# Optimization experiments

Hardware: AMD Instinct MI355X
Metric: run time of the kernel (lower is better)

The kernel has to match this reference:

```python
import jax, jax.numpy as jnp
import numpy as np
from jax import lax

OBS, ACT, H, VOX = 2264, 32, 4096, 216  # voxel tail is 6*6*6


def _conv3d(v, w, b):
    # v: [1,1,6,6,6], w: [1,1,3,3,3] (OIDHW), SAME padding, stride 1
    y = lax.conv_general_dilated(v, w, window_strides=(1, 1, 1), padding='SAME',
                                 dimension_numbers=('NCDHW', 'OIDHW', 'NCDHW'))
    return jax.nn.relu(y + b.reshape(1, -1, 1, 1, 1))


def setup_inputs() -> dict:
    key = jax.random.key(0)
    ks = jax.random.split(key, 24)
    s = 0.05
    inp = {'x': jax.random.normal(ks[0], (1, OBS), dtype=jnp.float32)}
    # six Conv3d(1,1,3) kernels + biases
    for i in range(6):
        inp[f'cw{i}'] = jax.random.normal(ks[1 + i], (1, 1, 3, 3, 3), dtype=jnp.float32) * s
        inp[f'cb{i}'] = jax.random.normal(ks[7 + i], (1,), dtype=jnp.float32) * s
    # MLP: Linear(OBS->H), Linear(H->H), Linear(H->ACT); torch layout W:[out,in]
    inp['W0'] = jax.random.normal(ks[13], (H, OBS), dtype=jnp.float32) * 0.02
    inp['b0'] = jnp.zeros((H,), jnp.float32)
    inp['W1'] = jax.random.normal(ks[14], (H, H), dtype=jnp.float32) * 0.02
    inp['b1'] = jnp.zeros((H,), jnp.float32)
    inp['W2'] = jax.random.normal(ks[15], (ACT, H), dtype=jnp.float32) * 0.02
    inp['b2'] = jnp.zeros((ACT,), jnp.float32)
    # default transformations (in_shift=0, in_scale=1, out_shift=0, out_scale=1)
    inp['in_shift'] = jnp.zeros((OBS,), jnp.float32)
    inp['in_scale'] = jnp.ones((OBS,), jnp.float32)
    inp['out_shift'] = jnp.zeros((ACT,), jnp.float32)
    inp['out_scale'] = jnp.ones((ACT,), jnp.float32)
    return inp


def reference(x, cw0, cw1, cw2, cw3, cw4, cw5, cb0, cb1, cb2, cb3, cb4, cb5,
              W0, b0, W1, b1, W2, b2, in_shift, in_scale, out_shift, out_scale):
    v = x[:, -VOX:].reshape(1, 1, 6, 6, 6)
    for w, b in ((cw0, cb0), (cw1, cb1), (cw2, cb2), (cw3, cb3), (cw4, cb4), (cw5, cb5)):
        v = _conv3d(v, w, b)
    out = jnp.concatenate([x[:, :-VOX], v.reshape(1, VOX)], axis=1)
    out = (out - in_shift) / (in_scale + 1e-8)
    out = jnp.tanh(out @ W0.T + b0)
    out = jnp.tanh(out @ W1.T + b1)
    out = out @ W2.T + b2
    return out * out_scale + out_shift
```

## Files before the change

kernel.cpp:

```cpp
#include <hip/hip_runtime.h>
#include <math.h>

#define OBS 2264
#define ACT 32
#define HID 4096
#define VOX 216
#define PRE (OBS - VOX)
#define N4_OBS (OBS / 4)
#define N4_HID (HID / 4)
#define ROWS0 8
#define ROWS1 4

__global__ __launch_bounds__(256) void conv_norm_kernel(
    const float* __restrict__ x,
    const float* __restrict__ cw0, const float* __restrict__ cb0,
    const float* __restrict__ cw1, const float* __restrict__ cb1,
    const float* __restrict__ cw2, const float* __restrict__ cb2,
    const float* __restrict__ cw3, const float* __restrict__ cb3,
    const float* __restrict__ cw4, const float* __restrict__ cb4,
    const float* __restrict__ cw5, const float* __restrict__ cb5,
    const float* __restrict__ in_shift, const float* __restrict__ in_scale,
    float* __restrict__ u)
{
    __shared__ float skw[6][27];
    __shared__ float skb[6];
    __shared__ float vbA[VOX], vbB[VOX];

    const int tid = threadIdx.x;

    if (tid < 162) {
        const float* srcw = tid < 27  ? cw0
                          : tid < 54  ? cw1
                          : tid < 81  ? cw2
                          : tid < 108 ? cw3
                          : tid < 135 ? cw4 : cw5;
        const int base = tid < 27  ? 0
                       : tid < 54  ? 27
                       : tid < 81  ? 54
                       : tid < 108 ? 81
                       : tid < 135 ? 108 : 135;
        reinterpret_cast<float*>(skw)[tid] = srcw[tid - base];
    } else if (tid >= 192 && tid < 198) {
        const float* srcb = tid == 192 ? cb0
                          : tid == 193 ? cb1
                          : tid == 194 ? cb2
                          : tid == 195 ? cb3
                          : tid == 196 ? cb4 : cb5;
        skb[tid - 192] = srcb[0];
    }
    if (tid < VOX) vbA[tid] = x[PRE + tid];
    __syncthreads();

    const int d = tid / 36;
    const int h = (tid / 6) % 6;
    const int w = tid % 6;

#define CONV_LAYER(L, SRC, DST)                                              \
    if (tid < VOX) {                                                         \
        float acc = skb[L];                                                  \
        _Pragma("unroll") for (int kd = 0; kd < 3; ++kd) {                   \
            const int dd = d + kd - 1;                                       \
            if (dd >= 0 && dd <= 5) {                                        \
                _Pragma("unroll") for (int kh = 0; kh < 3; ++kh) {           \
                    const int hh = h + kh - 1;                               \
                    if (hh >= 0 && hh <= 5) {                                \
                        _Pragma("unroll") for (int kw2 = 0; kw2 < 3; ++kw2) {\
                            const int ww = w + kw2 - 1;                      \
                            if (ww >= 0 && ww <= 5)                          \
                                acc += skw[L][kd * 9 + kh * 3 + kw2]         \
                                     * SRC[dd * 36 + hh * 6 + ww];           \
                        }                                                    \
                    }                                                        \
                }                                                            \
            }                                                                \
        }                                                                    \
        DST[tid] = fmaxf(acc, 0.f);                                          \
    }                                                                        \
    __syncthreads();

    CONV_LAYER(0, vbA, vbB)
    CONV_LAYER(1, vbB, vbA)
    CONV_LAYER(2, vbA, vbB)
    CONV_LAYER(3, vbB, vbA)
    CONV_LAYER(4, vbA, vbB)
    CONV_LAYER(5, vbB, vbA)
#undef CONV_LAYER

    for (int i = tid; i < OBS; i += 256) {
        const float val = (i < PRE) ? x[i] : vbA[i - PRE];
        u[i] = (val - in_shift[i]) / (in_scale[i] + 1e-8f);
    }
}

__global__ __launch_bounds__(256) void gemv0_kernel(
    const float* __restrict__ W, const float* __restrict__ b,
    const float* __restrict__ u, float* __restrict__ out)
{
    const int row0 = blockIdx.x * ROWS0;
    const int tid = threadIdx.x;
    const float4* __restrict__ u4 = reinterpret_cast<const float4*>(u);
    const float4* __restrict__ W4 = reinterpret_cast<const float4*>(W);

    float accs[ROWS0];
    #pragma unroll
    for (int r = 0; r < ROWS0; ++r) accs[r] = 0.f;

    for (int j = tid; j < N4_OBS; j += 256) {
        const float4 uv = u4[j];
        #pragma unroll
        for (int r = 0; r < ROWS0; ++r) {
            const float4 wv = W4[(size_t)(row0 + r) * N4_OBS + j];
            accs[r] += wv.x * uv.x + wv.y * uv.y + wv.z * uv.z + wv.w * uv.w;
        }
    }

    __shared__ float part[ROWS0][4];
    #pragma unroll
    for (int r = 0; r < ROWS0; ++r) {
        float a = accs[r];
        #pragma unroll
        for (int off = 32; off > 0; off >>= 1) a += __shfl_down(a, off, 64);
        if ((tid & 63) == 0) part[r][tid >> 6] = a;
    }
    __syncthreads();
    if (tid < ROWS0) {
        const float s = part[tid][0] + part[tid][1] + part[tid][2] + part[tid][3]
                      + b[row0 + tid];
        out[row0 + tid] = tanhf(s);
    }
}

__global__ __launch_bounds__(256) void gemv1_kernel(
    const float* __restrict__ W, const float* __restrict__ b,
    const float* __restrict__ u, float* __restrict__ out)
{
    const int row0 = blockIdx.x * ROWS1;
    const int tid = threadIdx.x;
    const float4* __restrict__ u4 = reinterpret_cast<const float4*>(u);
    const float4* __restrict__ W4 = reinterpret_cast<const float4*>(W);

    float accs[ROWS1] = {0.f, 0.f, 0.f, 0.f};
    for (int j = tid; j < N4_HID; j += 256) {
        const float4 uv = u4[j];
        #pragma unroll
        for (int r = 0; r < ROWS1; ++r) {
            const float4 wv = W4[(size_t)(row0 + r) * N4_HID + j];
            accs[r] += wv.x * uv.x + wv.y * uv.y + wv.z * uv.z + wv.w * uv.w;
        }
    }
    __shared__ float part[ROWS1][4];
    #pragma unroll
    for (int r = 0; r < ROWS1; ++r) {
        float a = accs[r];
        #pragma unroll
        for (int off = 32; off > 0; off >>= 1) a += __shfl_down(a, off, 64);
        if ((tid & 63) == 0) part[r][tid >> 6] = a;
    }
    __syncthreads();
    if (tid < ROWS1) {
        const float s = part[tid][0] + part[tid][1] + part[tid][2] + part[tid][3]
                      + b[row0 + tid];
        out[row0 + tid] = tanhf(s);
    }
}

__global__ __launch_bounds__(1024) void gemv_out_kernel(
    const float* __restrict__ W, const float* __restrict__ b,
    const float* __restrict__ u,
    const float* __restrict__ oscale, const float* __restrict__ oshift,
    float* __restrict__ out)
{
    const int row = blockIdx.x;
    const int tid = threadIdx.x;
    const float4* __restrict__ Wr = reinterpret_cast<const float4*>(W + (size_t)row * HID);
    const float4* __restrict__ u4 = reinterpret_cast<const float4*>(u);

    const float4 wv = Wr[tid];
    const float4 uv = u4[tid];
    float a = wv.x * uv.x + wv.y * uv.y + wv.z * uv.z + wv.w * uv.w;

    #pragma unroll
    for (int off = 32; off > 0; off >>= 1) a += __shfl_down(a, off, 64);

    __shared__ float part[16];
    if ((tid & 63) == 0) part[tid >> 6] = a;
    __syncthreads();
    if (tid == 0) {
        float s = b[row];
        #pragma unroll
        for (int i = 0; i < 16; ++i) s += part[i];
        out[row] = s * oscale[row] + oshift[row];
    }
}

extern "C" void kernel_launch(void* const* d_in, const int* in_sizes, int n_in,
                              void* d_out, int out_size, void* d_ws, size_t ws_size,
                              hipStream_t stream) {
    const float* x = (const float*)d_in[0];

    const float* cw[6];
    const float* cb[6];
    if (in_sizes[2] == 1) {
        for (int i = 0; i < 6; ++i) {
            cw[i] = (const float*)d_in[1 + 2 * i];
            cb[i] = (const float*)d_in[2 + 2 * i];
        }
    } else {
        for (int i = 0; i < 6; ++i) {
            cw[i] = (const float*)d_in[1 + i];
            cb[i] = (const float*)d_in[7 + i];
        }
    }
    const float* W0       = (const float*)d_in[13];
    const float* b0       = (const float*)d_in[14];
    const float* W1       = (const float*)d_in[15];
    const float* b1       = (const float*)d_in[16];
    const float* W2       = (const float*)d_in[17];
    const float* b2       = (const float*)d_in[18];
    const float* in_shift = (const float*)d_in[19];
    const float* in_scale = (const float*)d_in[20];
    const float* oshift   = (const float*)d_in[21];
    const float* oscale   = (const float*)d_in[22];

    float* ws = (float*)d_ws;
    float* u  = ws;
    float* h0 = ws + 2304;
    float* h1 = ws + 6400;
    float* y  = (float*)d_out;

    conv_norm_kernel<<<1, 256, 0, stream>>>(
        x, cw[0], cb[0], cw[1], cb[1], cw[2], cb[2],
        cw[3], cb[3], cw[4], cb[4], cw[5], cb[5],
        in_shift, in_scale, u);

    gemv0_kernel<<<HID / ROWS0, 256, 0, stream>>>(W0, b0, u, h0);
    gemv1_kernel<<<HID / ROWS1, 256, 0, stream>>>(W1, b1, h0, h1);
    gemv_out_kernel<<<ACT, 1024, 0, stream>>>(W2, b2, h1, oscale, oshift, y);
}
```

Before: 41.26 us.

## Fuse conv and three GEMVs into one persistent kernel with grid barriers

Replaces the four kernel launches with a single persistent kernel of 256 blocks of 1024 threads that synchronise through an atomic grid barrier in workspace memory. Each block redundantly computes the tiny 3D conv and normalization into shared memory, then runs its slice of each GEMV. The aim is to remove the launch gaps and the serial single-block conv stage. The cost is a memset before launch, redundant conv work in every block, barrier spin latency, and a deadlock risk if not all 256 blocks are co-resident.

```diff
diff --git a/kernel.cpp b/kernel.cpp
--- a/kernel.cpp
+++ b/kernel.cpp
@@ -8,10 +8,30 @@
 #define PRE (OBS - VOX)
 #define N4_OBS (OBS / 4)
 #define N4_HID (HID / 4)
-#define ROWS0 8
-#define ROWS1 4
-
-__global__ __launch_bounds__(256) void conv_norm_kernel(
+#define NB 256
+#define NT 1024
+#define RPB 16
+#define RPG 4
+
+__device__ __forceinline__ void grid_barrier(unsigned* cnt, int tid) {
+    __syncthreads();
+    if (tid == 0) {
+        __threadfence();
+        const unsigned old = __hip_atomic_fetch_add(cnt, 1u, __ATOMIC_ACQ_REL,
+                                                    __HIP_MEMORY_SCOPE_AGENT);
+        const unsigned target = (old / NB + 1u) * NB;
+        unsigned guard = 0;
+        while (__hip_atomic_load(cnt, __ATOMIC_ACQUIRE,
+                                 __HIP_MEMORY_SCOPE_AGENT) < target) {
+            __builtin_amdgcn_s_sleep(2);
+            if (++guard > (1u << 24)) break;
+        }
+        __threadfence();
+    }
+    __syncthreads();
+}
+
+__global__ __launch_bounds__(NT) void persistent_kernel(
     const float* __restrict__ x,
     const float* __restrict__ cw0, const float* __restrict__ cb0,
     const float* __restrict__ cw1, const float* __restrict__ cb1,
@@ -20,11 +40,20 @@
     const float* __restrict__ cw4, const float* __restrict__ cb4,
     const float* __restrict__ cw5, const float* __restrict__ cb5,
     const float* __restrict__ in_shift, const float* __restrict__ in_scale,
-    float* __restrict__ u)
+    const float* __restrict__ W0, const float* __restrict__ b0,
+    const float* __restrict__ W1, const float* __restrict__ b1,
+    const float* __restrict__ W2, const float* __restrict__ b2,
+    const float* __restrict__ oscale, const float* __restrict__ oshift,
+    unsigned* __restrict__ bar,
+    float* __restrict__ h0, float* __restrict__ h1,
+    float* __restrict__ y)
 {
     __shared__ float skw[6][27];
     __shared__ float skb[6];
     __shared__ float vbA[VOX], vbB[VOX];
+    __shared__ __align__(16) float su[OBS];
+    __shared__ float part[4][RPG][4];
+    __shared__ float part16[16];
 
     const int tid = threadIdx.x;
 
@@ -86,110 +115,93 @@
     CONV_LAYER(5, vbB, vbA)
 #undef CONV_LAYER
 
-    for (int i = tid; i < OBS; i += 256) {
+    for (int i = tid; i < OBS; i += NT) {
         const float val = (i < PRE) ? x[i] : vbA[i - PRE];
-        u[i] = (val - in_shift[i]) / (in_scale[i] + 1e-8f);
-    }
-}
-
-__global__ __launch_bounds__(256) void gemv0_kernel(
-    const float* __restrict__ W, const float* __restrict__ b,
-    const float* __restrict__ u, float* __restrict__ out)
-{
-    const int row0 = blockIdx.x * ROWS0;
-    const int tid = threadIdx.x;
-    const float4* __restrict__ u4 = reinterpret_cast<const float4*>(u);
-    const float4* __restrict__ W4 = reinterpret_cast<const float4*>(W);
-
-    float accs[ROWS0];
-    #pragma unroll
-    for (int r = 0; r < ROWS0; ++r) accs[r] = 0.f;
-
-    for (int j = tid; j < N4_OBS; j += 256) {
-        const float4 uv = u4[j];
+        su[i] = (val - in_shift[i]) / (in_scale[i] + 1e-8f);
+    }
+    __syncthreads();
+
+    const int g = tid >> 8;
+    const int t = tid & 255;
+
+    {
+        const int r0 = blockIdx.x * RPB + g * RPG;
+        const float4* __restrict__ su4 = reinterpret_cast<const float4*>(su);
+        const float4* __restrict__ W4  = reinterpret_cast<const float4*>(W0);
+        float accs[RPG] = {0.f, 0.f, 0.f, 0.f};
+        for (int j = t; j < N4_OBS; j += 256) {
+            const float4 uv = su4[j];
+            #pragma unroll
+            for (int r = 0; r < RPG; ++r) {
+                const float4 wv = W4[(size_t)(r0 + r) * N4_OBS + j];
+                accs[r] += wv.x * uv.x + wv.y * uv.y + wv.z * uv.z + wv.w * uv.w;
+            }
+        }
         #pragma unroll
-        for (int r = 0; r < ROWS0; ++r) {
-            const float4 wv = W4[(size_t)(row0 + r) * N4_OBS + j];
-            accs[r] += wv.x * uv.x + wv.y * uv.y + wv.z * uv.z + wv.w * uv.w;
-        }
-    }
-
-    __shared__ float part[ROWS0][4];
-    #pragma unroll
-    for (int r = 0; r < ROWS0; ++r) {
-        float a = accs[r];
+        for (int r = 0; r < RPG; ++r) {
+            float a = accs[r];
+            #pragma unroll
+            for (int off = 32; off > 0; off >>= 1) a += __shfl_down(a, off, 64);
+            if ((t & 63) == 0) part[g][r][t >> 6] = a;
+        }
+        __syncthreads();
+        if (t < RPG) {
+            const float s = part[g][t][0] + part[g][t][1] + part[g][t][2]
+                          + part[g][t][3] + b0[r0 + t];
+            h0[r0 + t] = tanhf(s);
+        }
+    }
+
+    grid_barrier(bar, tid);
+
+    {
+        const int r0 = blockIdx.x * RPB + g * RPG;
+        const float4* __restrict__ u4 = reinterpret_cast<const float4*>(h0);
+        const float4* __restrict__ W4 = reinterpret_cast<const float4*>(W1);
+        float accs[RPG] = {0.f, 0.f, 0.f, 0.f};
+        for (int j = t; j < N4_HID; j += 256) {
+            const float4 uv = u4[j];
+            #pragma unroll
+            for (int r = 0; r < RPG; ++r) {
+                const float4 wv = W4[(size_t)(r0 + r) * N4_HID + j];
+                accs[r] += wv.x * uv.x + wv.y * uv.y + wv.z * uv.z + wv.w * uv.w;
+            }
+        }
+        #pragma unroll
+        for (int r = 0; r < RPG; ++r) {
+            float a = accs[r];
+            #pragma unroll
+            for (int off = 32; off > 0; off >>= 1) a += __shfl_down(a, off, 64);
+            if ((t & 63) == 0) part[g][r][t >> 6] = a;
+        }
+        __syncthreads();
+        if (t < RPG) {
+            const float s = part[g][t][0] + part[g][t][1] + part[g][t][2]
+                          + part[g][t][3] + b1[r0 + t];
+            h1[r0 + t] = tanhf(s);
+        }
+    }
+
+    grid_barrier(bar, tid);
+
+    if (blockIdx.x < ACT) {
+        const int row = blockIdx.x;
+        const float4* __restrict__ Wr =
+            reinterpret_cast<const float4*>(W2 + (size_t)row * HID);
+        const float4* __restrict__ u4 = reinterpret_cast<const float4*>(h1);
+        const float4 wv = Wr[tid];
+        const float4 uv = u4[tid];
+        float a = wv.x * uv.x + wv.y * uv.y + wv.z * uv.z + wv.w * uv.w;
         #pragma unroll
         for (int off = 32; off > 0; off >>= 1) a += __shfl_down(a, off, 64);
-        if ((tid & 63) == 0) part[r][tid >> 6] = a;
-    }
-    __syncthreads();
-    if (tid < ROWS0) {
-        const float s = part[tid][0] + part[tid][1] + part[tid][2] + part[tid][3]
-                      + b[row0 + tid];
-        out[row0 + tid] = tanhf(s);
-    }
-}
-
-__global__ __launch_bounds__(256) void gemv1_kernel(
-    const float* __restrict__ W, const float* __restrict__ b,
-    const float* __restrict__ u, float* __restrict__ out)
-{
-    const int row0 = blockIdx.x * ROWS1;
-    const int tid = threadIdx.x;
-    const float4* __restrict__ u4 = reinterpret_cast<const float4*>(u);
-    const float4* __restrict__ W4 = reinterpret_cast<const float4*>(W);
-
-    float accs[ROWS1] = {0.f, 0.f, 0.f, 0.f};
-    for (int j = tid; j < N4_HID; j += 256) {
-        const float4 uv = u4[j];
-        #pragma unroll
-        for (int r = 0; r < ROWS1; ++r) {
-            const float4 wv = W4[(size_t)(row0 + r) * N4_HID + j];
-            accs[r] += wv.x * uv.x + wv.y * uv.y + wv.z * uv.z + wv.w * uv.w;
-        }
-    }
-    __shared__ float part[ROWS1][4];
-    #pragma unroll
-    for (int r = 0; r < ROWS1; ++r) {
-        float a = accs[r];
-        #pragma unroll
-        for (int off = 32; off > 0; off >>= 1) a += __shfl_down(a, off, 64);
-        if ((tid & 63) == 0) part[r][tid >> 6] = a;
-    }
-    __syncthreads();
-    if (tid < ROWS1) {
-        const float s = part[tid][0] + part[tid][1] + part[tid][2] + part[tid][3]
-                      + b[row0 + tid];
-        out[row0 + tid] = tanhf(s);
-    }
-}
-
-__global__ __launch_bounds__(1024) void gemv_out_kernel(
-    const float* __restrict__ W, const float* __restrict__ b,
-    const float* __restrict__ u,
-    const float* __restrict__ oscale, const float* __restrict__ oshift,
-    float* __restrict__ out)
-{
-    const int row = blockIdx.x;
-    const int tid = threadIdx.x;
-    const float4* __restrict__ Wr = reinterpret_cast<const float4*>(W + (size_t)row * HID);
-    const float4* __restrict__ u4 = reinterpret_cast<const float4*>(u);
-
-    const float4 wv = Wr[tid];
-    const float4 uv = u4[tid];
-    float a = wv.x * uv.x + wv.y * uv.y + wv.z * uv.z + wv.w * uv.w;
-
-    #pragma unroll
-    for (int off = 32; off > 0; off >>= 1) a += __shfl_down(a, off, 64);
-
-    __shared__ float part[16];
-    if ((tid & 63) == 0) part[tid >> 6] = a;
-    __syncthreads();
-    if (tid == 0) {
-        float s = b[row];
-        #pragma unroll
-        for (int i = 0; i < 16; ++i) s += part[i];
-        out[row] = s * oscale[row] + oshift[row];
+        if ((tid & 63) == 0) part16[tid >> 6] = a;
+        __syncthreads();
+        if (tid == 0) {
+            float s = b2[row];
+            #pragma unroll
+            for (int i = 0; i < 16; ++i) s += part16[i];
+            y[row] = s * oscale[row] + oshift[row];
+        }
     }
 }
 
@@ -222,18 +234,17 @@
     const float* oshift   = (const float*)d_in[21];
     const float* oscale   = (const float*)d_in[22];
 
-    float* ws = (float*)d_ws;
-    float* u  = ws;
-    float* h0 = ws + 2304;
-    float* h1 = ws + 6400;
-    float* y  = (float*)d_out;
-
-    conv_norm_kernel<<<1, 256, 0, stream>>>(
+    unsigned* bar = (unsigned*)d_ws;
+    float*    wsf = (float*)d_ws;
+    float*    h0  = wsf + 64;
+    float*    h1  = wsf + 64 + HID;
+    float*    y   = (float*)d_out;
+
+    hipMemsetAsync(d_ws, 0, 256, stream);
+
+    persistent_kernel<<<NB, NT, 0, stream>>>(
         x, cw[0], cb[0], cw[1], cb[1], cw[2], cb[2],
         cw[3], cb[3], cw[4], cb[4], cw[5], cb[5],
-        in_shift, in_scale, u);
-
-    gemv0_kernel<<<HID / ROWS0, 256, 0, stream>>>(W0, b0, u, h0);
-    gemv1_kernel<<<HID / ROWS1, 256, 0, stream>>>(W1, b1, h0, h1);
-    gemv_out_kernel<<<ACT, 1024, 0, stream>>>(W2, b2, h1, oscale, oshift, y);
+        in_shift, in_scale, W0, b0, W1, b1, W2, b2,
+        oscale, oshift, bar, h0, h1, y);
 }
```

Result: slower. 81.13 us (+96.6%).
